# Optimization experiments

Hardware: AMD Instinct MI355X
Metric: run time of the kernel (lower is better)

The kernel has to match this reference:

```python
import jax, jax.numpy as jnp
import numpy as np

H = 4                      # attention heads
L_NAMES = ['self', 'cross'] * 3
K_LIST = [None, None, 128, 128, 64, 64]  # top-k per layer (None = full attention)
BN_EPS = 1e-5


def conv1d(x, W, b):
    # 1x1 Conv1d: x [B, Ci, N], W [Co, Ci], b [Co]
    return jnp.einsum('oi,bin->bon', W, x) + b[:, None]


def bn_eval(x, g, b):
    # BatchNorm1d in eval mode with running mean 0 / var 1
    inv = 1.0 / np.sqrt(1.0 + BN_EPS)
    return (g * inv)[:, None] * x + b[:, None]


def mha(x, src, Wq, bq, Wk, bk, Wv, bv, Wm, bm, k):
    B, D, N = x.shape
    dh = D // H
    q = conv1d(x, Wq, bq).reshape(B, dh, H, N)
    kk = conv1d(src, Wk, bk).reshape(B, dh, H, -1)
    v = conv1d(src, Wv, bv).reshape(B, dh, H, -1)
    scores = jnp.einsum('bdhn,bdhm->bhnm', q, kk) / np.sqrt(dh)  # [B,H,N,M]
    if k is None:
        p = jax.nn.softmax(scores, axis=-1)
        out = jnp.einsum('bhnm,bdhm->bdhn', p, v)
    else:
        vals, idx = jax.lax.top_k(scores, k)          # [B,H,N,k]
        S = jax.nn.softmax(vals, axis=-1)
        # gather value vectors at the top-k key indices: [B,dh,H,N,k]
        vg = jnp.take_along_axis(v[:, :, :, None, :], idx[:, None, :, :, :], axis=4)
        out = jnp.einsum('bhnk,bdhnk->bdhn', S, vg)
    return conv1d(out.reshape(B, D, N), Wm, bm)


def log_ot(scores, alpha, iters):
    b, m, n = scores.shape
    bins0 = jnp.broadcast_to(alpha, (b, m, 1))
    bins1 = jnp.broadcast_to(alpha, (b, 1, n))
    a = jnp.broadcast_to(alpha, (b, 1, 1))
    Z0 = jnp.concatenate([jnp.concatenate([scores, bins0], -1),
                          jnp.concatenate([bins1, a], -1)], 1)  # [b,m+1,n+1]
    norm = -np.log(float(m + n))
    log_mu = jnp.concatenate([jnp.full((m,), norm, scores.dtype),
                              jnp.array([np.log(float(n)) + norm], scores.dtype)])
    log_nu = jnp.concatenate([jnp.full((n,), norm, scores.dtype),
                              jnp.array([np.log(float(m)) + norm], scores.dtype)])
    log_mu = jnp.broadcast_to(log_mu, (b, m + 1))
    log_nu = jnp.broadcast_to(log_nu, (b, n + 1))

    def step(carry, _):
        u, v = carry
        u = log_mu - jax.nn.logsumexp(Z0 + v[:, None, :], axis=2)
        v = log_nu - jax.nn.logsumexp(Z0 + u[:, :, None], axis=1)
        return (u, v), None

    (u, v), _ = jax.lax.scan(step, (jnp.zeros_like(log_mu), jnp.zeros_like(log_nu)),
                             None, length=iters)
    return Z0 + u[:, :, None] + v[:, None, :] - norm


def _forward(desc0, desc1, Wq, bq, Wk, bk, Wv, bv, Wm, bm,
             W1, b1, g1, be1, W2, b2, Wf, bf, alpha, iters):
    d0, d1 = desc0, desc1
    for i, (name, k) in enumerate(zip(L_NAMES, K_LIST)):
        s0, s1 = (d1, d0) if name == 'cross' else (d0, d1)

        def prop(x, src):
            msg = mha(x, src, Wq[i], bq[i], Wk[i], bk[i], Wv[i], bv[i], Wm[i], bm[i], k)
            h = jnp.concatenate([x, msg], axis=1)           # [B, 2D, N]
            h = jax.nn.relu(bn_eval(conv1d(h, W1[i], b1[i]), g1[i], be1[i]))
            return conv1d(h, W2[i], b2[i])

        dlt0, dlt1 = prop(d0, s0), prop(d1, s1)
        d0, d1 = d0 + dlt0, d1 + dlt1
    m0 = conv1d(d0, Wf, bf)
    m1 = conv1d(d1, Wf, bf)
    scores = jnp.einsum('bdn,bdm->bnm', m0, m1) / np.sqrt(m0.shape[1])
    return log_ot(scores, alpha, iters)


def setup_inputs() -> dict:
    B, D, N, L = 4, 128, 1024, 6
    key = jax.random.key(0)
    ks = jax.random.split(key, 20)

    def nrm(k, shape, s):
        return jax.random.normal(k, shape, jnp.float32) * s

    sw = 1.0 / np.sqrt(D)
    return {
        'desc0': nrm(ks[0], (B, D, N), 1.0),
        'desc1': nrm(ks[1], (B, D, N), 1.0),
        'Wq': nrm(ks[2], (L, D, D), sw), 'bq': jnp.zeros((L, D), jnp.float32),
        'Wk': nrm(ks[3], (L, D, D), sw), 'bk': jnp.zeros((L, D), jnp.float32),
        'Wv': nrm(ks[4], (L, D, D), sw), 'bv': jnp.zeros((L, D), jnp.float32),
        'Wm': nrm(ks[5], (L, D, D), sw), 'bm': jnp.zeros((L, D), jnp.float32),
        'W1': nrm(ks[6], (L, 2 * D, 2 * D), 1.0 / np.sqrt(2 * D)),
        'b1': jnp.zeros((L, 2 * D), jnp.float32),
        'g1': jnp.ones((L, 2 * D), jnp.float32),
        'be1': jnp.zeros((L, 2 * D), jnp.float32),
        'W2': nrm(ks[7], (L, D, 2 * D), 1.0 / np.sqrt(2 * D)),
        'b2': jnp.zeros((L, D), jnp.float32),
        'Wf': nrm(ks[8], (D, D), sw), 'bf': jnp.zeros((D,), jnp.float32),
        'alpha': jnp.asarray(1.0, jnp.float32),
        'iters': 20,
    }


def reference(desc0, desc1, Wq, bq, Wk, bk, Wv, bv, Wm, bm,
              W1, b1, g1, be1, W2, b2, Wf, bf, alpha, iters):
    return _forward(desc0, desc1, Wq, bq, Wk, bk, Wv, bv, Wm, bm,
                    W1, b1, g1, be1, W2, b2, Wf, bf, alpha, iters)
```

## Files before the change

kernel.cpp:

```cpp
#include <hip/hip_runtime.h>
#include <hip/hip_fp16.h>
#include <stdint.h>

#define NPOS   1024
#define DMODEL 128
#define NP1    1025
#define PLP    1053700
#define PSTR   1028
#define PLPH   1057800
#define PSTRH  1032
#define NORMF  (-7.624618986159398f)
#define LOGN   (6.931471805599453f)

typedef __attribute__((ext_vector_type(8))) short s8v;
typedef __attribute__((ext_vector_type(4))) float f4v;
typedef unsigned short ushort_t;

#define MFMA(a, b, c) __builtin_amdgcn_mfma_f32_16x16x32_bf16((a), (b), (c), 0, 0, 0)

static __device__ __forceinline__ ushort_t f2bf(float f) {
    union { float f; uint32_t u; } c; c.f = f;
    uint32_t u = c.u;
    return (ushort_t)((u + 0x7fffu + ((u >> 16) & 1u)) >> 16);
}
static __device__ __forceinline__ uint32_t cvtpk(float lo, float hi) {
    uint32_t r;
    asm("v_cvt_pk_bf16_f32 %0, %1, %2" : "=v"(r) : "v"(lo), "v"(hi));
    return r;
}

#define NW0 294912
#define NW2 393216
#define NW3 196608
#define NW4 16384
#define NB5 2304
#define NPREP (NW0 + NW2 + NW3 + NW4 + NB5)
__global__ __launch_bounds__(256) void prep_weights(
    const float* __restrict__ Wq, const float* __restrict__ Wk, const float* __restrict__ Wv,
    const float* __restrict__ bq, const float* __restrict__ bk, const float* __restrict__ bv,
    const float* __restrict__ W1, const float* __restrict__ W2, const float* __restrict__ Wf,
    ushort_t* __restrict__ wqkv, ushort_t* __restrict__ w1c,
    ushort_t* __restrict__ w2, ushort_t* __restrict__ wf, float* __restrict__ bqkv)
{
    int idx = blockIdx.x * 256 + threadIdx.x;
    if (idx < NW0) {
        int l = idx / 49152, r2 = idx % 49152;
        int r = r2 / 128, i = r2 % 128;
        int sel = r >> 7, rr = r & 127;
        int o = ((rr & 31) << 2) + (rr >> 5);
        const float* src = sel == 0 ? Wq : (sel == 1 ? Wk : Wv);
        wqkv[idx] = f2bf(src[((size_t)l * 128 + o) * 128 + i]);
        return;
    }
    idx -= NW0;
    if (idx < NW2) {
        int i = idx & 255;
        if (i < 128) w1c[idx] = f2bf(W1[idx]);
        return;
    }
    idx -= NW2;
    if (idx < NW3) { w2[idx] = f2bf(W2[idx]); return; }
    idx -= NW3;
    if (idx < NW4) { wf[idx] = f2bf(Wf[idx]); return; }
    idx -= NW4;
    if (idx < NB5) {
        int l = idx / 384, r = idx % 384;
        int sel = r >> 7, rr = r & 127;
        int o = ((rr & 31) << 2) + (rr >> 5);
        const float* src = sel == 0 ? bq : (sel == 1 ? bk : bv);
        bqkv[idx] = src[l * 128 + o];
    }
}

#define NFOLD 196608
#define NFB   1536
__global__ __launch_bounds__(256) void fold_w1(
    const float* __restrict__ W1, const float* __restrict__ Wm,
    const float* __restrict__ b1, const float* __restrict__ bm,
    ushort_t* __restrict__ w1c, float* __restrict__ b1c)
{
    int idx = blockIdx.x * 256 + threadIdx.x;
    if (idx < NFOLD) {
        int l = idx / 32768, rem = idx % 32768;
        int o = rem / 128, ip = rem % 128;
        int i = ((ip & 31) << 2) + (ip >> 5);
        const float* w1row = W1 + ((size_t)l * 256 + o) * 256 + 128;
        const float* wmcol = Wm + (size_t)l * 16384 + i;
        float s = 0.f;
        #pragma unroll 8
        for (int j = 0; j < 128; ++j) s = fmaf(w1row[j], wmcol[(size_t)j * 128], s);
        w1c[((size_t)l * 256 + o) * 256 + 128 + ip] = f2bf(s);
        return;
    }
    idx -= NFOLD;
    if (idx < NFB) {
        int l = idx / 256, o = idx % 256;
        const float* w1row = W1 + ((size_t)l * 256 + o) * 256 + 128;
        const float* bml = bm + l * 128;
        float s = b1[l * 256 + o];
        #pragma unroll 8
        for (int j = 0; j < 128; ++j) s = fmaf(w1row[j], bml[j], s);
        b1c[idx] = s;
    }
}

__global__ __launch_bounds__(256) void transpose_in(
    const float* __restrict__ desc0, const float* __restrict__ desc1,
    float* __restrict__ df, ushort_t* __restrict__ db)
{
    int g = blockIdx.z;
    int nb = blockIdx.x << 6, cb = blockIdx.y << 5;
    __shared__ float sm[32][65];
    const float* S = (g < 4 ? desc0 : desc1);
    int gl = g & 3;
    {
        int row = threadIdx.x >> 3, c8 = (threadIdx.x & 7) << 3;
        const float* p = S + ((size_t)gl * 128 + cb + row) * NPOS + nb + c8;
        float4 v0 = *(const float4*)p;
        float4 v1 = *(const float4*)(p + 4);
        sm[row][c8 + 0] = v0.x; sm[row][c8 + 1] = v0.y; sm[row][c8 + 2] = v0.z; sm[row][c8 + 3] = v0.w;
        sm[row][c8 + 4] = v1.x; sm[row][c8 + 5] = v1.y; sm[row][c8 + 6] = v1.z; sm[row][c8 + 7] = v1.w;
    }
    __syncthreads();
    int n = threadIdx.x >> 2, cc = (threadIdx.x & 3) << 3;
    float y[8];
    #pragma unroll
    for (int e = 0; e < 8; ++e) y[e] = sm[cc + e][n];
    size_t base = ((size_t)g * NPOS + nb + n) * DMODEL + cb + cc;
    *(float4*)(df + base) = make_float4(y[0], y[1], y[2], y[3]);
    *(float4*)(df + base + 4) = make_float4(y[4], y[5], y[6], y[7]);
    uint4 pk = make_uint4(cvtpk(y[0], y[1]), cvtpk(y[2], y[3]),
                          cvtpk(y[4], y[5]), cvtpk(y[6], y[7]));
    *(uint4*)(db + base) = pk;
}

__global__ __launch_bounds__(256) void conv_mfma(
    const ushort_t* __restrict__ X0, const ushort_t* __restrict__ X1, int c0, int Ci,
    const ushort_t* __restrict__ W, const float* __restrict__ bias,
    const float* __restrict__ bn_g, const float* __restrict__ bn_b,
    float* __restrict__ resid, ushort_t* __restrict__ outb, int Co, int mode)
{
    int g = blockIdx.z;
    int nb = blockIdx.x << 6;
    int obb = blockIdx.y << 6;
    int wave = threadIdx.x >> 6, lane = threadIdx.x & 63;
    int lrow = lane & 15, lk = (lane >> 4) << 3;
    int ob = obb + (wave << 4);
    f4v acc[4] = {};
    const ushort_t* wrow = W + (size_t)(ob + lrow) * Ci + lk;
    for (int k0 = 0; k0 < Ci; k0 += 32) {
        int k = k0 + lk;
        s8v b = *(const s8v*)(wrow + k0);
        #pragma unroll
        for (int t = 0; t < 4; ++t) {
            int n = nb + (t << 4) + lrow;
            const ushort_t* xp;
            if (k < c0) xp = X0 + ((size_t)g * NPOS + n) * c0 + k;
            else        xp = X1 + ((size_t)g * NPOS + n) * (Ci - c0) + (k - c0);
            s8v a = *(const s8v*)xp;
            acc[t] = MFMA(a, b, acc[t]);
        }
    }
    __shared__ float sm[64][68];
    #pragma unroll
    for (int t = 0; t < 4; ++t)
        #pragma unroll
        for (int r = 0; r < 4; ++r)
            sm[(t << 4) + ((lane >> 4) << 2) + r][(wave << 4) + lrow] = acc[t][r];
    __syncthreads();
    const float BN_INV = 0.9999950000374997f;
    int n = threadIdx.x >> 2, oc = (threadIdx.x & 3) << 4;
    int o0 = obb + oc;
    float y[16];
    #pragma unroll
    for (int e = 0; e < 16; ++e) y[e] = sm[n][oc + e] + bias[o0 + e];
    size_t base = ((size_t)g * NPOS + nb + n) * Co + o0;
    if (mode == 1) {
        #pragma unroll
        for (int e = 0; e < 16; ++e)
            y[e] = fmaxf(bn_g[o0 + e] * BN_INV * y[e] + bn_b[o0 + e], 0.f);
    } else if (mode == 2) {
        float* rp = resid + base;
        #pragma unroll
        for (int q = 0; q < 16; q += 4) {
            float4 r4 = *(const float4*)(rp + q);
            y[q] += r4.x; y[q + 1] += r4.y; y[q + 2] += r4.z; y[q + 3] += r4.w;
            *(float4*)(rp + q) = make_float4(y[q], y[q + 1], y[q + 2], y[q + 3]);
        }
    }
    uint4 p0 = make_uint4(cvtpk(y[0], y[1]), cvtpk(y[2], y[3]),
                          cvtpk(y[4], y[5]), cvtpk(y[6], y[7]));
    uint4 p1 = make_uint4(cvtpk(y[8], y[9]), cvtpk(y[10], y[11]),
                          cvtpk(y[12], y[13]), cvtpk(y[14], y[15]));
    *(uint4*)(outb + base) = p0;
    *(uint4*)(outb + base + 8) = p1;
}

__global__ __launch_bounds__(256) void qkv_mfma(
    const ushort_t* __restrict__ X, const ushort_t* __restrict__ W,
    const float* __restrict__ bias,
    ushort_t* __restrict__ Qb, ushort_t* __restrict__ Kb, ushort_t* __restrict__ Vb)
{
    int g = blockIdx.z;
    int nb = blockIdx.x << 6;
    int obb = blockIdx.y << 6;
    int wave = threadIdx.x >> 6, lane = threadIdx.x & 63;
    int lrow = lane & 15, lk = (lane >> 4) << 3;
    int ob = obb + (wave << 4);
    f4v acc[4] = {};
    const ushort_t* wrow = W + (size_t)(ob + lrow) * DMODEL + lk;
    for (int k0 = 0; k0 < DMODEL; k0 += 32) {
        s8v b = *(const s8v*)(wrow + k0);
        #pragma unroll
        for (int t = 0; t < 4; ++t) {
            int n = nb + (t << 4) + lrow;
            s8v a = *(const s8v*)(X + ((size_t)g * NPOS + n) * DMODEL + k0 + lk);
            acc[t] = MFMA(a, b, acc[t]);
        }
    }
    __shared__ float sm[64][68];
    #pragma unroll
    for (int t = 0; t < 4; ++t)
        #pragma unroll
        for (int r = 0; r < 4; ++r)
            sm[(t << 4) + ((lane >> 4) << 2) + r][(wave << 4) + lrow] = acc[t][r];
    __syncthreads();
    if (obb < 256) {
        int n = threadIdx.x >> 2, oc = (threadIdx.x & 3) << 4;
        int ov = obb + oc;
        ushort_t* dst = (ov < 128) ? Qb : Kb;
        int c = ov & 127;
        float y[16];
        #pragma unroll
        for (int e = 0; e < 16; ++e) y[e] = sm[n][oc + e] + bias[ov + e];
        size_t base = ((size_t)g * NPOS + nb + n) * DMODEL + c;
        uint4 p0 = make_uint4(cvtpk(y[0], y[1]), cvtpk(y[2], y[3]),
                              cvtpk(y[4], y[5]), cvtpk(y[6], y[7]));
        uint4 p1 = make_uint4(cvtpk(y[8], y[9]), cvtpk(y[10], y[11]),
                              cvtpk(y[12], y[13]), cvtpk(y[14], y[15]));
        *(uint4*)(dst + base) = p0;
        *(uint4*)(dst + base + 8) = p1;
    } else {
        int c = threadIdx.x >> 2, mc = (threadIdx.x & 3) << 4;
        float bc = bias[obb + c];
        float y[16];
        #pragma unroll
        for (int e = 0; e < 16; ++e) y[e] = sm[mc + e][c] + bc;
        size_t base = ((size_t)g * DMODEL + (obb - 256) + c) * NPOS + nb + mc;
        uint4 p0 = make_uint4(cvtpk(y[0], y[1]), cvtpk(y[2], y[3]),
                              cvtpk(y[4], y[5]), cvtpk(y[6], y[7]));
        uint4 p1 = make_uint4(cvtpk(y[8], y[9]), cvtpk(y[10], y[11]),
                              cvtpk(y[12], y[13]), cvtpk(y[14], y[15]));
        *(uint4*)(Vb + base) = p0;
        *(uint4*)(Vb + base + 8) = p1;
    }
}

__global__ __launch_bounds__(256) void attn_fused(
    const ushort_t* __restrict__ Qb, const ushort_t* __restrict__ Kb,
    const ushort_t* __restrict__ Vb, ushort_t* __restrict__ ao,
    int k, int cross)
{
    __shared__ ushort_t sc[16 * 1024];
    int gh = blockIdx.y;
    int g = gh >> 2, h = gh & 3;
    int g2 = cross ? (g ^ 4) : g;
    int n0 = blockIdx.x << 4;
    int wave = threadIdx.x >> 6, lane = threadIdx.x & 63;
    int lrow = lane & 15, lq = lane >> 4;

    {
        int kq = wave;
        s8v qa = *(const s8v*)(Qb + ((size_t)g * NPOS + n0 + lrow) * DMODEL
                               + (h << 5) + (lq << 3));
        const float scale = 0.17677669529663687f;
        int swz = (lrow & 7) << 4;
        for (int mt = 0; mt < 16; ++mt) {
            int m = (kq << 8) + (mt << 4);
            s8v kb = *(const s8v*)(Kb + ((size_t)g2 * NPOS + m + lrow) * DMODEL
                                   + (h << 5) + (lq << 3));
            f4v z = {};
            z = MFMA(kb, qa, z);
            uint32_t p0 = cvtpk(z[0] * scale, z[1] * scale);
            uint32_t p1 = cvtpk(z[2] * scale, z[3] * scale);
            int byte = ((lrow << 11) + ((m + (lq << 2)) << 1)) ^ swz;
            *(uint2*)((char*)sc + byte) = make_uint2(p0, p1);
        }
    }

    int khalf = wave >> 1, dimg = wave & 1;
    const ushort_t* vbase = Vb + ((size_t)g2 * DMODEL + (h << 5) + (dimg << 4) + lrow) * NPOS
                            + (khalf << 9) + (lq << 3);
    s8v vpre[8];
    #pragma unroll
    for (int ks = 0; ks < 8; ++ks) vpre[ks] = *(const s8v*)(vbase + (ks << 5));

    __syncthreads();

    {
        bool dosel = (k < NPOS);
        for (int rr = 0; rr < 4; ++rr) {
            int row = (wave << 2) + rr;
            int swz = (row & 7) << 4;
            int base = (row << 11) + (lane << 5);
            uint4 d0 = *(const uint4*)((const char*)sc + (base ^ swz));
            uint4 d1 = *(const uint4*)((const char*)sc + ((base + 16) ^ swz));
            uint32_t wd[8] = {d0.x, d0.y, d0.z, d0.w, d1.x, d1.y, d1.z, d1.w};
            float val[16];
            #pragma unroll
            for (int q = 0; q < 8; ++q) {
                union { unsigned ui; float f; } c0, c1;
                c0.ui = wd[q] << 16; c1.ui = wd[q] & 0xFFFF0000u;
                val[2 * q] = c0.f; val[2 * q + 1] = c1.f;
            }
            float mx = val[0];
            #pragma unroll
            for (int t = 1; t < 16; ++t) mx = fmaxf(mx, val[t]);
            #pragma unroll
            for (int o = 32; o; o >>= 1) mx = fmaxf(mx, __shfl_xor(mx, o));

            bool sel[16];
            if (dosel) {
                unsigned prefix = 0;
                bool exact = false;
                for (int bit = 15; bit >= 0 && !exact; --bit) {
                    unsigned cand = prefix | (1u << bit);
                    unsigned craw = (cand & 0x8000u) ? (cand ^ 0x8000u) : (cand ^ 0xFFFFu);
                    union { unsigned ui; float f; } cf; cf.ui = craw << 16;
                    float cf_f = cf.f;
                    int c = 0;
                    #pragma unroll
                    for (int t = 0; t < 16; ++t)
                        c += __popcll(__ballot(val[t] >= cf_f));
                    if (c >= k) { prefix = cand; exact = (c == k); }
                }
                unsigned praw = (prefix & 0x8000u) ? (prefix ^ 0x8000u) : (prefix ^ 0xFFFFu);
                union { unsigned ui; float f; } pf; pf.ui = praw << 16;
                float thr = pf.f;
                if (exact) {
                    #pragma unroll
                    for (int t = 0; t < 16; ++t) sel[t] = (val[t] >= thr);
                } else {
                    int cgt = 0;
                    #pragma unroll
                    for (int t = 0; t < 16; ++t)
                        cgt += __popcll(__ballot(val[t] > thr));
                    int need = k - cgt;
                    unsigned long long lmask = (1ull << lane) - 1ull;
                    int before = 0;
                    #pragma unroll
                    for (int t = 0; t < 16; ++t)
                        before += __popcll(__ballot(val[t] == thr) & lmask);
                    int loc = 0;
                    #pragma unroll
                    for (int t = 0; t < 16; ++t) {
                        bool tie = (val[t] == thr);
                        sel[t] = (val[t] > thr) || (tie && (before + loc < need));
                        loc += tie ? 1 : 0;
                    }
                }
            } else {
                #pragma unroll
                for (int t = 0; t < 16; ++t) sel[t] = true;
            }
            float w[16], sum = 0.f;
            #pragma unroll
            for (int t = 0; t < 16; ++t) {
                w[t] = sel[t] ? __expf(val[t] - mx) : 0.f;
                sum += w[t];
            }
            #pragma unroll
            for (int o = 32; o; o >>= 1) sum += __shfl_xor(sum, o);
            float inv = 1.f / sum;
            uint32_t ow[8];
            #pragma unroll
            for (int q = 0; q < 8; ++q)
                ow[q] = cvtpk(w[2 * q] * inv, w[2 * q + 1] * inv);
            *(uint4*)((char*)sc + (base ^ swz)) = make_uint4(ow[0], ow[1], ow[2], ow[3]);
            *(uint4*)((char*)sc + ((base + 16) ^ swz)) = make_uint4(ow[4], ow[5], ow[6], ow[7]);
        }
    }
    __syncthreads();

    {
        int db = dimg << 4;
        int pswz = (lrow & 7) << 4;
        int pbase = (lrow << 11) + (khalf << 10) + (lq << 4);
        f4v acc = {};
        #pragma unroll
        for (int ks = 0; ks < 8; ++ks) {
            s8v pa = *(const s8v*)((const char*)sc + ((pbase + (ks << 6)) ^ pswz));
            acc = MFMA(pa, vpre[ks], acc);
        }
        #pragma unroll
        for (int ks = 8; ks < 16; ++ks) {
            s8v pa = *(const s8v*)((const char*)sc + ((pbase + (ks << 6)) ^ pswz));
            s8v vv = *(const s8v*)(vbase + (ks << 5));
            acc = MFMA(pa, vv, acc);
        }
        __syncthreads();
        if (khalf == 1)
            *(f4v*)((char*)sc + (((dimg << 6) + lane) << 4)) = acc;
        __syncthreads();
        if (khalf == 0) {
            f4v other = *(const f4v*)((char*)sc + (((dimg << 6) + lane) << 4));
            acc = acc + other;
            #pragma unroll
            for (int r = 0; r < 4; ++r) {
                int n = n0 + (lq << 2) + r;
                ao[((size_t)g * NPOS + n) * DMODEL + (h << 5) + db + lrow] = f2bf(acc[r]);
            }
        }
    }
}

__global__ __launch_bounds__(256) void final_mfma(
    const ushort_t* __restrict__ md, float* __restrict__ Z0P,
    __half* __restrict__ Z0H, __half* __restrict__ Z0TH)
{
    int b = blockIdx.z;
    int wave = threadIdx.x >> 6, lane = threadIdx.x & 63;
    int wr = wave >> 1, wc = wave & 1;
    int n0 = (blockIdx.y << 7) + (wr << 6);
    int m0 = (blockIdx.x << 7) + (wc << 6);
    int lrow = lane & 15, lk = (lane >> 4) << 3;
    f4v acc[4][4] = {};
    for (int k0 = 0; k0 < DMODEL; k0 += 32) {
        s8v qa[4], kb[4];
        #pragma unroll
        for (int t = 0; t < 4; ++t) {
            qa[t] = *(const s8v*)(md + ((size_t)b * NPOS + n0 + (t << 4) + lrow) * DMODEL + k0 + lk);
            kb[t] = *(const s8v*)(md + ((size_t)(b + 4) * NPOS + m0 + (t << 4) + lrow) * DMODEL + k0 + lk);
        }
        #pragma unroll
        for (int tn = 0; tn < 4; ++tn)
            #pragma unroll
            for (int tm = 0; tm < 4; ++tm)
                acc[tn][tm] = MFMA(qa[tn], kb[tm], acc[tn][tm]);
    }
    const float scf = 0.08838834764831845f;
    int rbase = (lane >> 4) << 2;
    #pragma unroll
    for (int tn = 0; tn < 4; ++tn) {
        #pragma unroll
        for (int tm = 0; tm < 4; ++tm) {
            #pragma unroll
            for (int r = 0; r < 4; ++r) {
                int n = n0 + (tn << 4) + rbase + r;
                int m = m0 + (tm << 4) + lrow;
                float y = acc[tn][tm][r] * scf;
                Z0P[(size_t)b * PLP + (size_t)n * PSTR + m] = y;
                __half hy = __float2half(y);
                Z0H [(size_t)b * PLPH + (size_t)n * PSTRH + m] = hy;
                Z0TH[(size_t)b * PLPH + (size_t)m * PSTRH + n] = hy;
            }
        }
    }
}

__global__ __launch_bounds__(1024) void ot_init(
    float* __restrict__ Z0P, __half* __restrict__ Z0H, __half* __restrict__ Z0TH,
    float* __restrict__ v, const float* __restrict__ alpha)
{
    float a = *alpha;
    __half ha = __float2half(a);
    int b = blockIdx.x, t = threadIdx.x;
    Z0P [(size_t)b * PLP  + (size_t)t * PSTR  + 1024] = a;
    Z0P [(size_t)b * PLP  + (size_t)1024 * PSTR + t] = a;
    Z0H [(size_t)b * PLPH + (size_t)t * PSTRH + 1024] = ha;
    Z0H [(size_t)b * PLPH + (size_t)1024 * PSTRH + t] = ha;
    Z0TH[(size_t)b * PLPH + (size_t)t * PSTRH + 1024] = ha;
    Z0TH[(size_t)b * PLPH + (size_t)1024 * PSTRH + t] = ha;
    v[b * NP1 + t] = 0.f;
    if (t == 0) {
        Z0P [(size_t)b * PLP  + (size_t)1024 * PSTR  + 1024] = a;
        Z0H [(size_t)b * PLPH + (size_t)1024 * PSTRH + 1024] = ha;
        Z0TH[(size_t)b * PLPH + (size_t)1024 * PSTRH + 1024] = ha;
        v[b * NP1 + 1024] = 0.f;
    }
}

__global__ __launch_bounds__(256) void lse_sweep_h(
    const __half* __restrict__ Z, const float* __restrict__ vin,
    float* __restrict__ uout)
{
    int wv = threadIdx.x >> 6, lane = threadIdx.x & 63;
    int r = blockIdx.x * 4 + wv;
    int b = r / NP1, i = r - b * NP1;
    const __half* z  = Z + (size_t)b * PLPH + (size_t)i * PSTRH;
    const float* vb = vin + b * NP1;
    float x[17];
    #pragma unroll
    for (int t = 0; t < 2; ++t) {
        int j = (t << 9) + (lane << 3);
        union { uint4 u; __half h[8]; } U;
        U.u = *(const uint4*)(z + j);
        float4 v0 = *(const float4*)(vb + j);
        float4 v1 = *(const float4*)(vb + j + 4);
        x[t * 8 + 0] = __half2float(U.h[0]) + v0.x;
        x[t * 8 + 1] = __half2float(U.h[1]) + v0.y;
        x[t * 8 + 2] = __half2float(U.h[2]) + v0.z;
        x[t * 8 + 3] = __half2float(U.h[3]) + v0.w;
        x[t * 8 + 4] = __half2float(U.h[4]) + v1.x;
        x[t * 8 + 5] = __half2float(U.h[5]) + v1.y;
        x[t * 8 + 6] = __half2float(U.h[6]) + v1.z;
        x[t * 8 + 7] = __half2float(U.h[7]) + v1.w;
    }
    x[16] = (lane == 0) ? (__half2float(z[1024]) + vb[1024]) : -1e30f;
    float m = x[0];
    #pragma unroll
    for (int t = 1; t < 17; ++t) m = fmaxf(m, x[t]);
    #pragma unroll
    for (int o = 32; o; o >>= 1) m = fmaxf(m, __shfl_xor(m, o));
    float sum = 0.f;
    #pragma unroll
    for (int t = 0; t < 17; ++t) sum += __expf(x[t] - m);
    #pragma unroll
    for (int o = 32; o; o >>= 1) sum += __shfl_xor(sum, o);
    if (lane == 0)
        uout[b * NP1 + i] = NORMF + ((i == 1024) ? LOGN : 0.f) - (m + __logf(sum));
}

__global__ __launch_bounds__(256) void ot_final(
    float* __restrict__ out, const float* __restrict__ Z0P,
    const float* __restrict__ u, const float* __restrict__ v)
{
    int r = blockIdx.x;
    int b = r / NP1, i = r - b * NP1;
    float ui = u[b * NP1 + i] - NORMF;
    const float* zp = Z0P + (size_t)b * PLP + (size_t)i * PSTR;
    float* zo = out + ((size_t)b * NP1 + i) * NP1;
    const float* vb = v + b * NP1;
    for (int j = threadIdx.x; j < NP1; j += 256) zo[j] = zp[j] + ui + vb[j];
}

extern "C" void kernel_launch(void* const* d_in, const int* in_sizes, int n_in,
                              void* d_out, int out_size, void* d_ws, size_t ws_size,
                              hipStream_t stream)
{
    (void)in_sizes; (void)n_in; (void)out_size; (void)ws_size;
    const float* desc0 = (const float*)d_in[0];
    const float* desc1 = (const float*)d_in[1];
    const float* Wq = (const float*)d_in[2];  const float* bq = (const float*)d_in[3];
    const float* Wk = (const float*)d_in[4];  const float* bk = (const float*)d_in[5];
    const float* Wv = (const float*)d_in[6];  const float* bv = (const float*)d_in[7];
    const float* Wm = (const float*)d_in[8];  const float* bm = (const float*)d_in[9];
    const float* W1 = (const float*)d_in[10]; const float* b1 = (const float*)d_in[11];
    const float* g1 = (const float*)d_in[12]; const float* be1 = (const float*)d_in[13];
    const float* W2 = (const float*)d_in[14]; const float* b2 = (const float*)d_in[15];
    const float* Wf = (const float*)d_in[16]; const float* bf = (const float*)d_in[17];
    const float* alpha = (const float*)d_in[18];

    float* Zout = (float*)d_out;
    float* ws = (float*)d_ws;
    size_t o = 0;
    float* d_f32      = ws;                          o += 1048576;
    ushort_t* d_bf    = (ushort_t*)(ws + o);         o += 524288;
    ushort_t* Qb      = (ushort_t*)(ws + o);         o += 524288;
    ushort_t* Kb      = (ushort_t*)(ws + o);         o += 524288;
    ushort_t* Vb      = (ushort_t*)(ws + o);         o += 524288;
    ushort_t* aob     = (ushort_t*)(ws + o);         o += 524288;
    ushort_t* hb      = (ushort_t*)(ws + o);         o += 1048576;
    ushort_t* mdesc   = (ushort_t*)(ws + o);         o += 524288;
    ushort_t* wqkv    = (ushort_t*)(ws + o);         o += 147456;
    ushort_t* w1c     = (ushort_t*)(ws + o);         o += 196608;
    ushort_t* w2w     = (ushort_t*)(ws + o);         o += 98304;
    ushort_t* wfw     = (ushort_t*)(ws + o);         o += 8192;
    float* bqkv       = ws + o;                      o += 2304;
    float* b1c        = ws + o;                      o += 1536;
    float* ub         = ws + o;                      o += 4352;
    float* vb         = ws + o;                      o += 4352;
    float* Z0P        = ws + o;                      o += 4214800;
    __half* Z0H       = (__half*)(ws + o);           o += 2115600;
    __half* Z0TH      = (__half*)(ws + o);           o += 2115600;

    dim3 blk(256);
    prep_weights<<<dim3((NPREP + 255) / 256), blk, 0, stream>>>(
        Wq, Wk, Wv, bq, bk, bv, W1, W2, Wf, wqkv, w1c, w2w, wfw, bqkv);
    fold_w1<<<dim3((NFOLD + NFB + 255) / 256), blk, 0, stream>>>(
        W1, Wm, b1, bm, w1c, b1c);
    transpose_in<<<dim3(16, 4, 8), blk, 0, stream>>>(desc0, desc1, d_f32, d_bf);

    static const int KLIST[6] = {1024, 1024, 128, 128, 64, 64};
    for (int l = 0; l < 6; ++l) {
        int cross = l & 1;
        int k = KLIST[l];
        qkv_mfma<<<dim3(16, 6, 8), blk, 0, stream>>>(
            d_bf, wqkv + (size_t)l * 49152, bqkv + l * 384, Qb, Kb, Vb);
        attn_fused<<<dim3(64, 32), blk, 0, stream>>>(Qb, Kb, Vb, aob, k, cross);
        conv_mfma<<<dim3(16, 4, 8), blk, 0, stream>>>(
            d_bf, aob, 128, 256, w1c + (size_t)l * 65536,
            b1c + l * 256, g1 + l * 256, be1 + l * 256, nullptr, hb, 256, 1);
        conv_mfma<<<dim3(16, 2, 8), blk, 0, stream>>>(
            hb, (const ushort_t*)nullptr, 256, 256, w2w + (size_t)l * 32768,
            b2 + l * 128, nullptr, nullptr, d_f32, d_bf, 128, 2);
    }
    conv_mfma<<<dim3(16, 2, 8), blk, 0, stream>>>(
        d_bf, (const ushort_t*)nullptr, 128, 128, wfw, bf,
        nullptr, nullptr, nullptr, mdesc, 128, 0);
    final_mfma<<<dim3(8, 8, 4), blk, 0, stream>>>(mdesc, Z0P, Z0H, Z0TH);
    ot_init<<<dim3(4), dim3(1024), 0, stream>>>(Z0P, Z0H, Z0TH, vb, alpha);
    for (int it = 0; it < 20; ++it) {
        lse_sweep_h<<<dim3(1025), blk, 0, stream>>>(Z0H,  vb, ub);
        lse_sweep_h<<<dim3(1025), blk, 0, stream>>>(Z0TH, ub, vb);
    }
    ot_final<<<dim3(4100), blk, 0, stream>>>(Zout, Z0P, ub, vb);
}
```

Baseline: 783.2 us.

## Raise attention occupancy, remap block ids, prefetch K, and interleave top-k rows

The attention kernel gets launch bounds that request four blocks per CU, trims the V prefetch from 8 to 4 registers, and software-pipelines the K tile loads four deep. The grid becomes 1-D, and block ids are remapped so that consecutive blocks cover different batch/head pairs, which spreads L2/XCD traffic. The top-k radix selection and softmax now process two rows at once so the ballot/shuffle chains of independent rows can overlap. The cost is more register pressure from the paired rows, which could cause spills under the tighter register budget.

```diff
diff --git a/kernel.cpp b/kernel.cpp
--- a/kernel.cpp
+++ b/kernel.cpp
@@ -256,16 +256,17 @@
     }
 }
 
-__global__ __launch_bounds__(256) void attn_fused(
+__global__ __launch_bounds__(256, 4) void attn_fused(
     const ushort_t* __restrict__ Qb, const ushort_t* __restrict__ Kb,
     const ushort_t* __restrict__ Vb, ushort_t* __restrict__ ao,
     int k, int cross)
 {
     __shared__ ushort_t sc[16 * 1024];
-    int gh = blockIdx.y;
+    int bid = blockIdx.x;
+    int gh = ((bid & 7) << 2) + (bid >> 9);
     int g = gh >> 2, h = gh & 3;
     int g2 = cross ? (g ^ 4) : g;
-    int n0 = blockIdx.x << 4;
+    int n0 = ((bid >> 3) & 63) << 4;
     int wave = threadIdx.x >> 6, lane = threadIdx.x & 63;
     int lrow = lane & 15, lq = lane >> 4;
 
@@ -275,109 +276,156 @@
                                + (h << 5) + (lq << 3));
         const float scale = 0.17677669529663687f;
         int swz = (lrow & 7) << 4;
+        const ushort_t* kb_base = Kb + ((size_t)g2 * NPOS + (kq << 8) + lrow) * DMODEL
+                                  + (h << 5) + (lq << 3);
+        #define KLOAD(mt) (*(const s8v*)(kb_base + (size_t)(mt) * 16 * DMODEL))
+        s8v kbuf[4];
+        #pragma unroll
+        for (int i = 0; i < 4; ++i) kbuf[i] = KLOAD(i);
+        #pragma unroll
         for (int mt = 0; mt < 16; ++mt) {
-            int m = (kq << 8) + (mt << 4);
-            s8v kb = *(const s8v*)(Kb + ((size_t)g2 * NPOS + m + lrow) * DMODEL
-                                   + (h << 5) + (lq << 3));
+            s8v kb = kbuf[mt & 3];
+            if (mt + 4 < 16) kbuf[mt & 3] = KLOAD(mt + 4);
             f4v z = {};
             z = MFMA(kb, qa, z);
             uint32_t p0 = cvtpk(z[0] * scale, z[1] * scale);
             uint32_t p1 = cvtpk(z[2] * scale, z[3] * scale);
+            int m = (kq << 8) + (mt << 4);
             int byte = ((lrow << 11) + ((m + (lq << 2)) << 1)) ^ swz;
             *(uint2*)((char*)sc + byte) = make_uint2(p0, p1);
         }
+        #undef KLOAD
     }
 
     int khalf = wave >> 1, dimg = wave & 1;
     const ushort_t* vbase = Vb + ((size_t)g2 * DMODEL + (h << 5) + (dimg << 4) + lrow) * NPOS
                             + (khalf << 9) + (lq << 3);
-    s8v vpre[8];
-    #pragma unroll
-    for (int ks = 0; ks < 8; ++ks) vpre[ks] = *(const s8v*)(vbase + (ks << 5));
+    s8v vpre[4];
+    #pragma unroll
+    for (int ks = 0; ks < 4; ++ks) vpre[ks] = *(const s8v*)(vbase + (ks << 5));
 
     __syncthreads();
 
     {
         bool dosel = (k < NPOS);
-        for (int rr = 0; rr < 4; ++rr) {
-            int row = (wave << 2) + rr;
-            int swz = (row & 7) << 4;
-            int base = (row << 11) + (lane << 5);
-            uint4 d0 = *(const uint4*)((const char*)sc + (base ^ swz));
-            uint4 d1 = *(const uint4*)((const char*)sc + ((base + 16) ^ swz));
-            uint32_t wd[8] = {d0.x, d0.y, d0.z, d0.w, d1.x, d1.y, d1.z, d1.w};
-            float val[16];
-            #pragma unroll
-            for (int q = 0; q < 8; ++q) {
-                union { unsigned ui; float f; } c0, c1;
-                c0.ui = wd[q] << 16; c1.ui = wd[q] & 0xFFFF0000u;
-                val[2 * q] = c0.f; val[2 * q + 1] = c1.f;
+        #pragma unroll
+        for (int pr = 0; pr < 2; ++pr) {
+            int row0 = (wave << 2) + (pr << 1);
+            uint32_t wd[2][8];
+            int swzr[2], baser[2];
+            #pragma unroll
+            for (int rp = 0; rp < 2; ++rp) {
+                int row = row0 + rp;
+                swzr[rp] = (row & 7) << 4;
+                baser[rp] = (row << 11) + (lane << 5);
+                uint4 d0 = *(const uint4*)((const char*)sc + (baser[rp] ^ swzr[rp]));
+                uint4 d1 = *(const uint4*)((const char*)sc + ((baser[rp] + 16) ^ swzr[rp]));
+                wd[rp][0] = d0.x; wd[rp][1] = d0.y; wd[rp][2] = d0.z; wd[rp][3] = d0.w;
+                wd[rp][4] = d1.x; wd[rp][5] = d1.y; wd[rp][6] = d1.z; wd[rp][7] = d1.w;
             }
-            float mx = val[0];
-            #pragma unroll
-            for (int t = 1; t < 16; ++t) mx = fmaxf(mx, val[t]);
-            #pragma unroll
-            for (int o = 32; o; o >>= 1) mx = fmaxf(mx, __shfl_xor(mx, o));
-
-            bool sel[16];
+            float val[2][16];
+            #pragma unroll
+            for (int rp = 0; rp < 2; ++rp)
+                #pragma unroll
+                for (int q = 0; q < 8; ++q) {
+                    union { unsigned ui; float f; } c0, c1;
+                    c0.ui = wd[rp][q] << 16; c1.ui = wd[rp][q] & 0xFFFF0000u;
+                    val[rp][2 * q] = c0.f; val[rp][2 * q + 1] = c1.f;
+                }
+            float mx[2];
+            #pragma unroll
+            for (int rp = 0; rp < 2; ++rp) {
+                mx[rp] = val[rp][0];
+                #pragma unroll
+                for (int t = 1; t < 16; ++t) mx[rp] = fmaxf(mx[rp], val[rp][t]);
+            }
+            #pragma unroll
+            for (int o = 32; o; o >>= 1)
+                #pragma unroll
+                for (int rp = 0; rp < 2; ++rp)
+                    mx[rp] = fmaxf(mx[rp], __shfl_xor(mx[rp], o));
+
+            bool sel[2][16];
             if (dosel) {
-                unsigned prefix = 0;
-                bool exact = false;
-                for (int bit = 15; bit >= 0 && !exact; --bit) {
-                    unsigned cand = prefix | (1u << bit);
-                    unsigned craw = (cand & 0x8000u) ? (cand ^ 0x8000u) : (cand ^ 0xFFFFu);
-                    union { unsigned ui; float f; } cf; cf.ui = craw << 16;
-                    float cf_f = cf.f;
-                    int c = 0;
+                unsigned prefix[2] = {0u, 0u};
+                bool exact[2] = {false, false};
+                for (int bit = 15; bit >= 0 && !(exact[0] && exact[1]); --bit) {
                     #pragma unroll
-                    for (int t = 0; t < 16; ++t)
-                        c += __popcll(__ballot(val[t] >= cf_f));
-                    if (c >= k) { prefix = cand; exact = (c == k); }
+                    for (int rp = 0; rp < 2; ++rp) {
+                        if (exact[rp]) continue;
+                        unsigned cand = prefix[rp] | (1u << bit);
+                        unsigned craw = (cand & 0x8000u) ? (cand ^ 0x8000u) : (cand ^ 0xFFFFu);
+                        union { unsigned ui; float f; } cf; cf.ui = craw << 16;
+                        float cf_f = cf.f;
+                        int c = 0;
+                        #pragma unroll
+                        for (int t = 0; t < 16; ++t)
+                            c += __popcll(__ballot(val[rp][t] >= cf_f));
+                        if (c >= k) { prefix[rp] = cand; exact[rp] = (c == k); }
+                    }
                 }
-                unsigned praw = (prefix & 0x8000u) ? (prefix ^ 0x8000u) : (prefix ^ 0xFFFFu);
-                union { unsigned ui; float f; } pf; pf.ui = praw << 16;
-                float thr = pf.f;
-                if (exact) {
-                    #pragma unroll
-                    for (int t = 0; t < 16; ++t) sel[t] = (val[t] >= thr);
-                } else {
-                    int cgt = 0;
-                    #pragma unroll
-                    for (int t = 0; t < 16; ++t)
-                        cgt += __popcll(__ballot(val[t] > thr));
-                    int need = k - cgt;
-                    unsigned long long lmask = (1ull << lane) - 1ull;
-                    int before = 0;
-                    #pragma unroll
-                    for (int t = 0; t < 16; ++t)
-                        before += __popcll(__ballot(val[t] == thr) & lmask);
-                    int loc = 0;
-                    #pragma unroll
-                    for (int t = 0; t < 16; ++t) {
-                        bool tie = (val[t] == thr);
-                        sel[t] = (val[t] > thr) || (tie && (before + loc < need));
-                        loc += tie ? 1 : 0;
+                #pragma unroll
+                for (int rp = 0; rp < 2; ++rp) {
+                    unsigned praw = (prefix[rp] & 0x8000u) ? (prefix[rp] ^ 0x8000u)
+                                                           : (prefix[rp] ^ 0xFFFFu);
+                    union { unsigned ui; float f; } pf; pf.ui = praw << 16;
+                    float thr = pf.f;
+                    if (exact[rp]) {
+                        #pragma unroll
+                        for (int t = 0; t < 16; ++t) sel[rp][t] = (val[rp][t] >= thr);
+                    } else {
+                        int cgt = 0;
+                        #pragma unroll
+                        for (int t = 0; t < 16; ++t)
+                            cgt += __popcll(__ballot(val[rp][t] > thr));
+                        int need = k - cgt;
+                        unsigned long long lmask = (1ull << lane) - 1ull;
+                        int before = 0;
+                        #pragma unroll
+                        for (int t = 0; t < 16; ++t)
+                            before += __popcll(__ballot(val[rp][t] == thr) & lmask);
+                        int loc = 0;
+                        #pragma unroll
+                        for (int t = 0; t < 16; ++t) {
+                            bool tie = (val[rp][t] == thr);
+                            sel[rp][t] = (val[rp][t] > thr) || (tie && (before + loc < need));
+                            loc += tie ? 1 : 0;
+                        }
                     }
                 }
             } else {
                 #pragma unroll
-                for (int t = 0; t < 16; ++t) sel[t] = true;
+                for (int rp = 0; rp < 2; ++rp)
+                    #pragma unroll
+                    for (int t = 0; t < 16; ++t) sel[rp][t] = true;
             }
-            float w[16], sum = 0.f;
-            #pragma unroll
-            for (int t = 0; t < 16; ++t) {
-                w[t] = sel[t] ? __expf(val[t] - mx) : 0.f;
-                sum += w[t];
+            float w[2][16], sum[2];
+            #pragma unroll
+            for (int rp = 0; rp < 2; ++rp) {
+                sum[rp] = 0.f;
+                #pragma unroll
+                for (int t = 0; t < 16; ++t) {
+                    w[rp][t] = sel[rp][t] ? __expf(val[rp][t] - mx[rp]) : 0.f;
+                    sum[rp] += w[rp][t];
+                }
             }
             #pragma unroll
-            for (int o = 32; o; o >>= 1) sum += __shfl_xor(sum, o);
-            float inv = 1.f / sum;
-            uint32_t ow[8];
-            #pragma unroll
-            for (int q = 0; q < 8; ++q)
-                ow[q] = cvtpk(w[2 * q] * inv, w[2 * q + 1] * inv);
-            *(uint4*)((char*)sc + (base ^ swz)) = make_uint4(ow[0], ow[1], ow[2], ow[3]);
-            *(uint4*)((char*)sc + ((base + 16) ^ swz)) = make_uint4(ow[4], ow[5], ow[6], ow[7]);
+            for (int o = 32; o; o >>= 1)
+                #pragma unroll
+                for (int rp = 0; rp < 2; ++rp)
+                    sum[rp] += __shfl_xor(sum[rp], o);
+            #pragma unroll
+            for (int rp = 0; rp < 2; ++rp) {
+                float inv = 1.f / sum[rp];
+                uint32_t ow[8];
+                #pragma unroll
+                for (int q = 0; q < 8; ++q)
+                    ow[q] = cvtpk(w[rp][2 * q] * inv, w[rp][2 * q + 1] * inv);
+                *(uint4*)((char*)sc + (baser[rp] ^ swzr[rp])) =
+                    make_uint4(ow[0], ow[1], ow[2], ow[3]);
+                *(uint4*)((char*)sc + ((baser[rp] + 16) ^ swzr[rp])) =
+                    make_uint4(ow[4], ow[5], ow[6], ow[7]);
+            }
         }
     }
     __syncthreads();
@@ -388,12 +436,12 @@
         int pbase = (lrow << 11) + (khalf << 10) + (lq << 4);
         f4v acc = {};
         #pragma unroll
-        for (int ks = 0; ks < 8; ++ks) {
+        for (int ks = 0; ks < 4; ++ks) {
             s8v pa = *(const s8v*)((const char*)sc + ((pbase + (ks << 6)) ^ pswz));
             acc = MFMA(pa, vpre[ks], acc);
         }
         #pragma unroll
-        for (int ks = 8; ks < 16; ++ks) {
+        for (int ks = 4; ks < 16; ++ks) {
             s8v pa = *(const s8v*)((const char*)sc + ((pbase + (ks << 6)) ^ pswz));
             s8v vv = *(const s8v*)(vbase + (ks << 5));
             acc = MFMA(pa, vv, acc);
@@ -587,7 +635,7 @@
         int k = KLIST[l];
         qkv_mfma<<<dim3(16, 6, 8), blk, 0, stream>>>(
             d_bf, wqkv + (size_t)l * 49152, bqkv + l * 384, Qb, Kb, Vb);
-        attn_fused<<<dim3(64, 32), blk, 0, stream>>>(Qb, Kb, Vb, aob, k, cross);
+        attn_fused<<<dim3(2048), blk, 0, stream>>>(Qb, Kb, Vb, aob, k, cross);
         conv_mfma<<<dim3(16, 4, 8), blk, 0, stream>>>(
             d_bf, aob, 128, 256, w1c + (size_t)l * 65536,
             b1c + l * 256, g1 + l * 256, be1 + l * 256, nullptr, hb, 256, 1);
```

Result: no change. 785.5 us (+0.3%).

## Double attention block to 512 threads with XCD-aware flat block remapping

Applied to the files above, without the earlier changes.

The attention kernel now runs 8 waves per block instead of 4. Each wave handles half as many score tiles, softmax rows and PV key chunks, and the PV partial sums are reduced across four key quarters through shared memory. The 2D grid becomes a flat 1D grid whose index is remapped so that consecutive blocks cycle over (batch, head) groups, likely to keep K/V for one head in the same XCD's L2. The V prefetch before the softmax phase is dropped, and the selection flags are packed into a bitmask to cut register use. The extra reduction round and the loss of V prefetch overlap may offset the gain in parallelism.

```diff
diff --git a/kernel.cpp b/kernel.cpp
--- a/kernel.cpp
+++ b/kernel.cpp
@@ -256,16 +256,17 @@
     }
 }
 
-__global__ __launch_bounds__(256) void attn_fused(
+__global__ __launch_bounds__(512, 8) void attn_fused(
     const ushort_t* __restrict__ Qb, const ushort_t* __restrict__ Kb,
     const ushort_t* __restrict__ Vb, ushort_t* __restrict__ ao,
     int k, int cross)
 {
     __shared__ ushort_t sc[16 * 1024];
-    int gh = blockIdx.y;
+    int bid = blockIdx.x;
+    int gh = ((bid & 7) << 2) + (bid >> 9);
     int g = gh >> 2, h = gh & 3;
     int g2 = cross ? (g ^ 4) : g;
-    int n0 = blockIdx.x << 4;
+    int n0 = ((bid >> 3) & 63) << 4;
     int wave = threadIdx.x >> 6, lane = threadIdx.x & 63;
     int lrow = lane & 15, lq = lane >> 4;
 
@@ -275,43 +276,39 @@
                                + (h << 5) + (lq << 3));
         const float scale = 0.17677669529663687f;
         int swz = (lrow & 7) << 4;
-        for (int mt = 0; mt < 16; ++mt) {
-            int m = (kq << 8) + (mt << 4);
-            s8v kb = *(const s8v*)(Kb + ((size_t)g2 * NPOS + m + lrow) * DMODEL
-                                   + (h << 5) + (lq << 3));
+        const ushort_t* kb_base = Kb + ((size_t)g2 * NPOS + (kq << 7) + lrow) * DMODEL
+                                  + (h << 5) + (lq << 3);
+        #pragma unroll
+        for (int mt = 0; mt < 8; ++mt) {
+            s8v kb = *(const s8v*)(kb_base + (size_t)mt * 16 * DMODEL);
             f4v z = {};
             z = MFMA(kb, qa, z);
             uint32_t p0 = cvtpk(z[0] * scale, z[1] * scale);
             uint32_t p1 = cvtpk(z[2] * scale, z[3] * scale);
+            int m = (kq << 7) + (mt << 4);
             int byte = ((lrow << 11) + ((m + (lq << 2)) << 1)) ^ swz;
             *(uint2*)((char*)sc + byte) = make_uint2(p0, p1);
         }
     }
-
-    int khalf = wave >> 1, dimg = wave & 1;
-    const ushort_t* vbase = Vb + ((size_t)g2 * DMODEL + (h << 5) + (dimg << 4) + lrow) * NPOS
-                            + (khalf << 9) + (lq << 3);
-    s8v vpre[8];
-    #pragma unroll
-    for (int ks = 0; ks < 8; ++ks) vpre[ks] = *(const s8v*)(vbase + (ks << 5));
-
     __syncthreads();
 
     {
         bool dosel = (k < NPOS);
-        for (int rr = 0; rr < 4; ++rr) {
-            int row = (wave << 2) + rr;
+        for (int rr = 0; rr < 2; ++rr) {
+            int row = (wave << 1) + rr;
             int swz = (row & 7) << 4;
             int base = (row << 11) + (lane << 5);
             uint4 d0 = *(const uint4*)((const char*)sc + (base ^ swz));
             uint4 d1 = *(const uint4*)((const char*)sc + ((base + 16) ^ swz));
-            uint32_t wd[8] = {d0.x, d0.y, d0.z, d0.w, d1.x, d1.y, d1.z, d1.w};
             float val[16];
-            #pragma unroll
-            for (int q = 0; q < 8; ++q) {
-                union { unsigned ui; float f; } c0, c1;
-                c0.ui = wd[q] << 16; c1.ui = wd[q] & 0xFFFF0000u;
-                val[2 * q] = c0.f; val[2 * q + 1] = c1.f;
+            {
+                uint32_t wd[8] = {d0.x, d0.y, d0.z, d0.w, d1.x, d1.y, d1.z, d1.w};
+                #pragma unroll
+                for (int q = 0; q < 8; ++q) {
+                    union { unsigned ui; float f; } c0, c1;
+                    c0.ui = wd[q] << 16; c1.ui = wd[q] & 0xFFFF0000u;
+                    val[2 * q] = c0.f; val[2 * q + 1] = c1.f;
+                }
             }
             float mx = val[0];
             #pragma unroll
@@ -319,7 +316,7 @@
             #pragma unroll
             for (int o = 32; o; o >>= 1) mx = fmaxf(mx, __shfl_xor(mx, o));
 
-            bool sel[16];
+            unsigned selmask = 0xFFFFu;
             if (dosel) {
                 unsigned prefix = 0;
                 bool exact = false;
@@ -338,8 +335,10 @@
                 union { unsigned ui; float f; } pf; pf.ui = praw << 16;
                 float thr = pf.f;
                 if (exact) {
+                    selmask = 0;
                     #pragma unroll
-                    for (int t = 0; t < 16; ++t) sel[t] = (val[t] >= thr);
+                    for (int t = 0; t < 16; ++t)
+                        selmask |= (val[t] >= thr) ? (1u << t) : 0u;
                 } else {
                     int cgt = 0;
                     #pragma unroll
@@ -352,22 +351,22 @@
                     for (int t = 0; t < 16; ++t)
                         before += __popcll(__ballot(val[t] == thr) & lmask);
                     int loc = 0;
+                    selmask = 0;
                     #pragma unroll
                     for (int t = 0; t < 16; ++t) {
                         bool tie = (val[t] == thr);
-                        sel[t] = (val[t] > thr) || (tie && (before + loc < need));
+                        if ((val[t] > thr) || (tie && (before + loc < need)))
+                            selmask |= (1u << t);
                         loc += tie ? 1 : 0;
                     }
                 }
-            } else {
-                #pragma unroll
-                for (int t = 0; t < 16; ++t) sel[t] = true;
             }
-            float w[16], sum = 0.f;
+            float sum = 0.f;
             #pragma unroll
             for (int t = 0; t < 16; ++t) {
-                w[t] = sel[t] ? __expf(val[t] - mx) : 0.f;
-                sum += w[t];
+                float wv = ((selmask >> t) & 1u) ? __expf(val[t] - mx) : 0.f;
+                val[t] = wv;
+                sum += wv;
             }
             #pragma unroll
             for (int o = 32; o; o >>= 1) sum += __shfl_xor(sum, o);
@@ -375,7 +374,7 @@
             uint32_t ow[8];
             #pragma unroll
             for (int q = 0; q < 8; ++q)
-                ow[q] = cvtpk(w[2 * q] * inv, w[2 * q + 1] * inv);
+                ow[q] = cvtpk(val[2 * q] * inv, val[2 * q + 1] * inv);
             *(uint4*)((char*)sc + (base ^ swz)) = make_uint4(ow[0], ow[1], ow[2], ow[3]);
             *(uint4*)((char*)sc + ((base + 16) ^ swz)) = make_uint4(ow[4], ow[5], ow[6], ow[7]);
         }
@@ -383,28 +382,27 @@
     __syncthreads();
 
     {
+        int kquad = wave >> 1, dimg = wave & 1;
         int db = dimg << 4;
+        const ushort_t* vbase = Vb + ((size_t)g2 * DMODEL + (h << 5) + db + lrow) * NPOS
+                                + (kquad << 8) + (lq << 3);
         int pswz = (lrow & 7) << 4;
-        int pbase = (lrow << 11) + (khalf << 10) + (lq << 4);
+        int pbase = (lrow << 11) + (kquad << 9) + (lq << 4);
         f4v acc = {};
         #pragma unroll
         for (int ks = 0; ks < 8; ++ks) {
-            s8v pa = *(const s8v*)((const char*)sc + ((pbase + (ks << 6)) ^ pswz));
-            acc = MFMA(pa, vpre[ks], acc);
-        }
-        #pragma unroll
-        for (int ks = 8; ks < 16; ++ks) {
             s8v pa = *(const s8v*)((const char*)sc + ((pbase + (ks << 6)) ^ pswz));
             s8v vv = *(const s8v*)(vbase + (ks << 5));
             acc = MFMA(pa, vv, acc);
         }
         __syncthreads();
-        if (khalf == 1)
-            *(f4v*)((char*)sc + (((dimg << 6) + lane) << 4)) = acc;
+        if (kquad > 0)
+            *(f4v*)((char*)sc + (((((kquad - 1) << 1) + dimg) * 64 + lane) << 4)) = acc;
         __syncthreads();
-        if (khalf == 0) {
-            f4v other = *(const f4v*)((char*)sc + (((dimg << 6) + lane) << 4));
-            acc = acc + other;
+        if (kquad == 0) {
+            #pragma unroll
+            for (int qq = 0; qq < 3; ++qq)
+                acc = acc + *(const f4v*)((char*)sc + ((((qq << 1) + dimg) * 64 + lane) << 4));
             #pragma unroll
             for (int r = 0; r < 4; ++r) {
                 int n = n0 + (lq << 2) + r;
@@ -587,7 +585,7 @@
         int k = KLIST[l];
         qkv_mfma<<<dim3(16, 6, 8), blk, 0, stream>>>(
             d_bf, wqkv + (size_t)l * 49152, bqkv + l * 384, Qb, Kb, Vb);
-        attn_fused<<<dim3(64, 32), blk, 0, stream>>>(Qb, Kb, Vb, aob, k, cross);
+        attn_fused<<<dim3(2048), dim3(512), 0, stream>>>(Qb, Kb, Vb, aob, k, cross);
         conv_mfma<<<dim3(16, 4, 8), blk, 0, stream>>>(
             d_bf, aob, 128, 256, w1c + (size_t)l * 65536,
             b1c + l * 256, g1 + l * 256, be1 + l * 256, nullptr, hb, 256, 1);
```

Result: faster. 746.0 us (-4.7%).
